# Kernel optimization log

Measured on AMD Instinct MI355X. Metric: run time of the kernel, lower is better.

Reference implementation:

```python
import jax, jax.numpy as jnp
import numpy as np

DIM = 256
KEY_DIM = 16
NUM_HEADS = 8
ATTN_RATIO = 4
NH_KD = KEY_DIM * NUM_HEADS   # 128
D = ATTN_RATIO * KEY_DIM      # 64
DH = D * NUM_HEADS            # 512
POS_LEN = 16
SCALE = KEY_DIM ** -0.5


def _cbn(x, w, s, b):
    # 1x1 conv (no bias) + folded BatchNorm affine. w: [out,in], x: [B,in,H,W]
    y = jnp.einsum('oi,bihw->bohw', w, x)
    return y * s[None, :, None, None] + b[None, :, None, None]


def _interp_pos(pos, n):
    # F.interpolate(mode='linear', align_corners=False) from length POS_LEN to n.
    L = pos.shape[-1]
    coords = (jnp.arange(n, dtype=pos.dtype) + 0.5) * (L / n) - 0.5
    coords = jnp.clip(coords, 0.0, L - 1)
    lo = jnp.floor(coords).astype(jnp.int32)
    hi = jnp.minimum(lo + 1, L - 1)
    t = coords - lo.astype(pos.dtype)
    return pos[..., lo] * (1 - t) + pos[..., hi] * t  # [1,C,n]


def _axial_attn(q_emb, k_emb, v_emb, pos_q, pos_k, n):
    # q_emb/k_emb: [B,NH_KD,n], v_emb: [B,DH,n]
    B = q_emb.shape[0]
    q = (q_emb + _interp_pos(pos_q, n)).reshape(B, NUM_HEADS, KEY_DIM, n)
    k = (k_emb + _interp_pos(pos_k, n)).reshape(B, NUM_HEADS, KEY_DIM, n)
    v = v_emb.reshape(B, NUM_HEADS, D, n)
    attn = jnp.einsum('bhcn,bhcm->bhnm', q, k) * SCALE
    attn = jax.nn.softmax(attn, axis=-1)
    xx = jnp.einsum('bhnm,bhdm->bhnd', attn, v)      # [B,NH,n,D]
    return xx.transpose(0, 1, 3, 2).reshape(B, DH, n)  # [B,DH,n]


def _forward(x, wq, sq, bq, wk, sk, bk, wv, sv, bv,
             pos_rowq, pos_rowk, pos_colq, pos_colk,
             w_row, s_row, b_row, w_col, s_col, b_col,
             w_proj, s_proj, b_proj, w_sc, s_sc, b_sc,
             w_dw, s_dw, b_dw, w_pw, s_pw, b_pw):
    B, C, H, W = x.shape
    q = _cbn(x, wq, sq, bq)   # [B,NH_KD,H,W]
    k = _cbn(x, wk, sk, bk)
    v = _cbn(x, wv, sv, bv)   # [B,DH,H,W]

    # row branch (mean over W)
    xx_row = _axial_attn(q.mean(-1), k.mean(-1), v.mean(-1), pos_rowq, pos_rowk, H)
    xx_row = _cbn(jax.nn.relu(xx_row[..., None]), w_row, s_row, b_row)      # [B,DH,H,1]
    # column branch (mean over H)
    xx_col = _axial_attn(q.mean(-2), k.mean(-2), v.mean(-2), pos_colq, pos_colk, W)
    xx_col = _cbn(jax.nn.relu(xx_col[:, :, None, :]), w_col, s_col, b_col)  # [B,DH,1,W]

    attn_out = v + (xx_row + xx_col)
    attn_out = _cbn(jax.nn.relu(attn_out), w_proj, s_proj, b_proj)          # [B,DIM,H,W]

    # gate branch: 1x1 -> dw3x3 -> relu -> 1x1 -> h_sigmoid
    gate = _cbn(x, w_sc, s_sc, b_sc)
    gate = jax.lax.conv_general_dilated(
        gate, w_dw, (1, 1), 'SAME',
        dimension_numbers=('NCHW', 'OIHW', 'NCHW'), feature_group_count=DIM)
    gate = gate * s_dw[None, :, None, None] + b_dw[None, :, None, None]
    gate = jax.nn.relu(gate)
    gate = _cbn(gate, w_pw, s_pw, b_pw)
    gate = jnp.clip(gate + 3.0, 0.0, 6.0) / 6.0  # h_sigmoid
    return gate * attn_out


def setup_inputs() -> dict:
    key = jax.random.key(0)
    ks = jax.random.split(key, 32)
    B, H, W = 16, 64, 64
    nrm = lambda k, sh, sc=0.05: jax.random.normal(k, sh, dtype=jnp.float32) * sc
    inp = {
        'x': nrm(ks[0], (B, DIM, H, W), 1.0),
        'wq': nrm(ks[1], (NH_KD, DIM)), 'sq': 1.0 + nrm(ks[2], (NH_KD,)), 'bq': nrm(ks[3], (NH_KD,)),
        'wk': nrm(ks[4], (NH_KD, DIM)), 'sk': 1.0 + nrm(ks[5], (NH_KD,)), 'bk': nrm(ks[6], (NH_KD,)),
        'wv': nrm(ks[7], (DH, DIM)), 'sv': 1.0 + nrm(ks[8], (DH,)), 'bv': nrm(ks[9], (DH,)),
        'pos_rowq': nrm(ks[10], (1, NH_KD, POS_LEN), 1.0), 'pos_rowk': nrm(ks[11], (1, NH_KD, POS_LEN), 1.0),
        'pos_colq': nrm(ks[12], (1, NH_KD, POS_LEN), 1.0), 'pos_colk': nrm(ks[13], (1, NH_KD, POS_LEN), 1.0),
        'w_row': nrm(ks[14], (DH, DH)), 's_row': 1.0 + nrm(ks[15], (DH,)), 'b_row': nrm(ks[16], (DH,)),
        'w_col': nrm(ks[17], (DH, DH)), 's_col': 1.0 + nrm(ks[18], (DH,)), 'b_col': nrm(ks[19], (DH,)),
        'w_proj': nrm(ks[20], (DIM, DH)), 's_proj': 1.0 + nrm(ks[21], (DIM,)), 'b_proj': nrm(ks[22], (DIM,)),
        'w_sc': nrm(ks[23], (DIM, DIM)), 's_sc': 1.0 + nrm(ks[24], (DIM,)), 'b_sc': nrm(ks[25], (DIM,)),
        'w_dw': nrm(ks[26], (DIM, 1, 3, 3)), 's_dw': 1.0 + nrm(ks[27], (DIM,)), 'b_dw': nrm(ks[28], (DIM,)),
        'w_pw': nrm(ks[29], (DIM, DIM)), 's_pw': 1.0 + nrm(ks[30], (DIM,)), 'b_pw': nrm(ks[31], (DIM,)),
    }
    return inp


def reference(x, wq, sq, bq, wk, sk, bk, wv, sv, bv,
              pos_rowq, pos_rowk, pos_colq, pos_colk,
              w_row, s_row, b_row, w_col, s_col, b_col,
              w_proj, s_proj, b_proj, w_sc, s_sc, b_sc,
              w_dw, s_dw, b_dw, w_pw, s_pw, b_pw):
    return _forward(x, wq, sq, bq, wk, sk, bk, wv, sv, bv,
                    pos_rowq, pos_rowk, pos_colq, pos_colk,
                    w_row, s_row, b_row, w_col, s_col, b_col,
                    w_proj, s_proj, b_proj, w_sc, s_sc, b_sc,
                    w_dw, s_dw, b_dw, w_pw, s_pw, b_pw)
```

## Files before the change

kernel.cpp:

```cpp
#include <hip/hip_runtime.h>
#include <math.h>

typedef unsigned short u16;
typedef unsigned int u32;
typedef short short8 __attribute__((ext_vector_type(8)));
typedef float f32x4 __attribute__((ext_vector_type(4)));

#define Bn 16
#define Cc 256
#define Pp 4096
#define DHc 512
#define PTOT 65536
#define SCALE 0.25f

__device__ __forceinline__ float bf2f(u16 u) {
    return __uint_as_float(((u32)u) << 16);
}
__device__ __forceinline__ u16 f2bf(float f) {
    u32 u = __float_as_uint(f);
    u32 lsb = (u >> 16) & 1u;
    u += 0x7fffu + lsb;
    return (u16)(u >> 16);
}

__device__ __forceinline__ void gload16(const u16* g, u16* l) {
    __builtin_amdgcn_global_load_lds(
        (const __attribute__((address_space(1))) void*)(uintptr_t)g,
        (__attribute__((address_space(3))) void*)(u32)(uintptr_t)l,
        16, 0, 0);
}

__global__ __launch_bounds__(256) void mean_kernel(
    const float* __restrict__ x, u16* __restrict__ xmb) {
    __shared__ float plane[64][65];
    int bc = blockIdx.x;
    int b = bc >> 8, c = bc & 255;
    const float* xp = x + (size_t)bc * Pp;
    int tid = threadIdx.x;
#pragma unroll
    for (int k = 0; k < 16; ++k) {
        int idx = tid + k * 256;
        plane[idx >> 6][idx & 63] = xp[idx];
    }
    __syncthreads();
    if (tid < 64) {
        float s = 0.f;
#pragma unroll
        for (int w = 0; w < 64; ++w) s += plane[tid][w];
        xmb[((size_t)b * 64 + tid) * 256 + c] = f2bf(s * (1.f / 64.f));
    } else if (tid < 128) {
        int w = tid - 64;
        float s = 0.f;
#pragma unroll
        for (int h = 0; h < 64; ++h) s += plane[h][w];
        xmb[((size_t)1024 + b * 64 + w) * 256 + c] = f2bf(s * (1.f / 64.f));
    }
}

__global__ __launch_bounds__(256) void xpose_kernel(
    const float* __restrict__ x, u16* __restrict__ xbf) {
    __shared__ float tile[64][65];
    int pb = blockIdx.x;
    int cb = blockIdx.y;
    int b = blockIdx.z;
    int t = threadIdx.x;
    int p_l = t & 63, c_q = t >> 6;
    const float* xp = x + ((size_t)b * Cc + cb * 64) * Pp + pb * 64;
#pragma unroll
    for (int rr = 0; rr < 16; ++rr) {
        int c_l = rr * 4 + c_q;
        tile[p_l][c_l] = xp[(size_t)c_l * Pp + p_l];
    }
    __syncthreads();
    int c_l2 = t & 63, p_q = t >> 6;
    u16* dst = xbf + ((size_t)b * Pp + pb * 64) * Cc + cb * 64;
#pragma unroll
    for (int rr = 0; rr < 16; ++rr) {
        int p_l2 = rr * 4 + p_q;
        dst[(size_t)p_l2 * Cc + c_l2] = f2bf(tile[p_l2][c_l2]);
    }
}

__global__ __launch_bounds__(256) void wconv_kernel(
    const float* __restrict__ wq, const float* __restrict__ wk, const float* __restrict__ wv,
    const float* __restrict__ wsc, const float* __restrict__ wproj, const float* __restrict__ wpw,
    const float* __restrict__ wrow, const float* __restrict__ wcol,
    const float* __restrict__ wdw,
    u16* __restrict__ wqkvb, u16* __restrict__ wscb,
    u16* __restrict__ wprojb, u16* __restrict__ wpwb,
    u16* __restrict__ wrb, u16* __restrict__ wcb, float* __restrict__ wdwT) {
    int t = blockIdx.x * 256 + threadIdx.x;
    if (t < 2304) wdwT[(t % 9) * 256 + (t / 9)] = wdw[t];
    if (t < 32768) wqkvb[t] = f2bf(wq[t]);
    else if (t < 65536) wqkvb[t] = f2bf(wk[t - 32768]);
    else if (t < 196608) wqkvb[t] = f2bf(wv[t - 65536]);
    else if (t < 262144) wscb[t - 196608] = f2bf(wsc[t - 196608]);
    else if (t < 393216) wprojb[t - 262144] = f2bf(wproj[t - 262144]);
    else if (t < 458752) wpwb[t - 393216] = f2bf(wpw[t - 393216]);
    else if (t < 720896) wrb[t - 458752] = f2bf(wrow[t - 458752]);
    else wcb[t - 720896] = f2bf(wcol[t - 720896]);
}

__device__ __forceinline__ void gemm_mainloop(
    const u16* __restrict__ W, const u16* __restrict__ X, int K,
    int o0, size_t prow0, u16* ldsA, u16* ldsB, f32x4 (&acc)[4][4]) {
    int t = threadIdx.x;
    int w = t >> 6, lane = t & 63;
    int sr = (w << 5) + (lane >> 2);
    int ks = (lane & 3) * 8;
    const u16* gA = W + (size_t)(o0 + sr) * K + ks;
    const u16* gB = X + (prow0 + sr) * K + ks;
    u16* lA = ldsA + sr * 32 + ks;
    u16* lB = ldsB + sr * 32 + ks;
    int wo = (w >> 1) * 64, wp = (w & 1) * 64;
    const u16* fA = ldsA + (wo + (lane & 15)) * 32 + ((lane >> 4) * 8);
    const u16* fB = ldsB + (wp + (lane & 15)) * 32 + ((lane >> 4) * 8);

    for (int k0 = 0; k0 < K; k0 += 32) {
        if (k0) __syncthreads();
        gload16(gA + k0, lA);
        gload16(gA + k0 + (size_t)16 * K, lA + 16 * 32);
        gload16(gB + k0, lB);
        gload16(gB + k0 + (size_t)16 * K, lB + 16 * 32);
        __syncthreads();
        short8 a[4], b[4];
#pragma unroll
        for (int i = 0; i < 4; ++i) a[i] = *(const short8*)(fA + i * 16 * 32);
#pragma unroll
        for (int j = 0; j < 4; ++j) b[j] = *(const short8*)(fB + j * 16 * 32);
#pragma unroll
        for (int i = 0; i < 4; ++i)
#pragma unroll
            for (int j = 0; j < 4; ++j)
                acc[i][j] = __builtin_amdgcn_mfma_f32_16x16x32_bf16(a[i], b[j], acc[i][j], 0, 0, 0);
    }
}

__global__ __launch_bounds__(256) void gemm_qkv(
    const u16* __restrict__ Wb, const u16* __restrict__ X,
    const float* __restrict__ sq, const float* __restrict__ bq,
    const float* __restrict__ sk, const float* __restrict__ bk,
    const float* __restrict__ sv, const float* __restrict__ bv,
    const float* __restrict__ posrq, const float* __restrict__ posrk,
    const float* __restrict__ poscq, const float* __restrict__ posck,
    float* __restrict__ qrow, float* __restrict__ krow, float* __restrict__ vrow,
    float* __restrict__ qcol, float* __restrict__ kcol, float* __restrict__ vcol) {
    __shared__ u16 ldsA[128 * 32];
    __shared__ u16 ldsB[128 * 32];
    f32x4 acc[4][4];
#pragma unroll
    for (int i = 0; i < 4; ++i)
#pragma unroll
        for (int j = 0; j < 4; ++j) acc[i][j] = (f32x4){0.f, 0.f, 0.f, 0.f};
    int o0 = blockIdx.x * 128;
    size_t prow0 = (size_t)blockIdx.y * 128;
    gemm_mainloop(Wb, X, 256, o0, prow0, ldsA, ldsB, acc);

    int lane = threadIdx.x & 63, w = threadIdx.x >> 6;
    int wo = (w >> 1) * 64, wp = (w & 1) * 64;
    int quad = lane >> 4, cn = lane & 15;
#pragma unroll
    for (int j = 0; j < 4; ++j) {
        int p = (int)prow0 + wp + j * 16 + cn;
        int branch = p >> 10, loc = p & 1023;
        int b = loc >> 6, n = loc & 63;
        float coords = 0.25f * (float)n - 0.375f;
        coords = fminf(fmaxf(coords, 0.f), 15.f);
        int lo = (int)floorf(coords);
        int hi = min(lo + 1, 15);
        float tt = coords - (float)lo;
#pragma unroll
        for (int i = 0; i < 4; ++i) {
            int o = o0 + wo + i * 16 + quad * 4;
            if (o < 128) {
                const float* pos = branch ? poscq : posrq;
                float* dst = branch ? qcol : qrow;
#pragma unroll
                for (int r = 0; r < 4; ++r) {
                    int c = o + r;
                    float pv = pos[c * 16 + lo] * (1.f - tt) + pos[c * 16 + hi] * tt;
                    dst[b * 8192 + c * 64 + n] = acc[i][j][r] * sq[c] + bq[c] + pv;
                }
            } else if (o < 256) {
                const float* pos = branch ? posck : posrk;
                float* dst = branch ? kcol : krow;
#pragma unroll
                for (int r = 0; r < 4; ++r) {
                    int c = o - 128 + r;
                    float pv = pos[c * 16 + lo] * (1.f - tt) + pos[c * 16 + hi] * tt;
                    dst[b * 8192 + c * 64 + n] = acc[i][j][r] * sk[c] + bk[c] + pv;
                }
            } else {
                float* dst = branch ? vcol : vrow;
#pragma unroll
                for (int r = 0; r < 4; ++r) {
                    int c = o - 256 + r;
                    dst[b * 32768 + c * 64 + n] = acc[i][j][r] * sv[c] + bv[c];
                }
            }
        }
    }
}

__global__ __launch_bounds__(512, 2) void attn_kernel(
    const float* __restrict__ qr, const float* __restrict__ kr, const float* __restrict__ vr,
    const float* __restrict__ qc, const float* __restrict__ kc, const float* __restrict__ vc,
    u16* __restrict__ xxbf) {
    int branch = blockIdx.y;
    const float* q = branch ? qc : qr;
    const float* k = branch ? kc : kr;
    const float* v = branch ? vc : vr;
    int bh = blockIdx.x;
    int b = bh >> 3, h = bh & 7;
    __shared__ float qs[16][64], ks[16][64], vs[64][64];
    __shared__ float sl[64][65], el[64][65];
    int t = threadIdx.x;
#pragma unroll
    for (int i = t; i < 1024; i += 512) {
        int c = i >> 6, nn = i & 63;
        qs[c][nn] = q[b * 8192 + (h * 16 + c) * 64 + nn];
        ks[c][nn] = k[b * 8192 + (h * 16 + c) * 64 + nn];
    }
#pragma unroll
    for (int i = t; i < 4096; i += 512) {
        int d = i >> 6, nn = i & 63;
        vs[d][nn] = v[b * 32768 + (h * 64 + d) * 64 + nn];
    }
    __syncthreads();

    int n = t & 63, dq = t >> 6;
    float qv[16];
#pragma unroll
    for (int c = 0; c < 16; ++c) qv[c] = qs[c][n];

    float sp[8];
#pragma unroll
    for (int mm = 0; mm < 8; ++mm) {
        int m = dq * 8 + mm;
        float acc = 0.f;
#pragma unroll
        for (int c = 0; c < 16; ++c) acc += qv[c] * ks[c][m];
        sp[mm] = acc * SCALE;
        sl[n][m] = sp[mm];
    }
    __syncthreads();

    float mx = -1e30f;
#pragma unroll
    for (int m = 0; m < 64; ++m) mx = fmaxf(mx, sl[n][m]);

#pragma unroll
    for (int mm = 0; mm < 8; ++mm) el[n][dq * 8 + mm] = __expf(sp[mm] - mx);
    __syncthreads();

    float sum = 0.f;
#pragma unroll
    for (int m = 0; m < 64; ++m) sum += el[n][m];
    float inv = 1.f / sum;

    float acc[8];
#pragma unroll
    for (int dd = 0; dd < 8; ++dd) acc[dd] = 0.f;
#pragma unroll
    for (int m = 0; m < 64; ++m) {
        float e = el[n][m];
#pragma unroll
        for (int dd = 0; dd < 8; ++dd) acc[dd] += e * vs[dq * 8 + dd][m];
    }
    u16* dst = xxbf + (((size_t)(b * 2 + branch)) * 64 + n) * 512 + h * 64 + dq * 8;
#pragma unroll
    for (int dd = 0; dd < 8; ++dd)
        dst[dd] = f2bf(fmaxf(acc[dd] * inv, 0.f));
}

__global__ __launch_bounds__(256) void post_gemm(
    const u16* __restrict__ xxbf, const u16* __restrict__ wrb, const u16* __restrict__ wcb,
    const float* __restrict__ s_row, const float* __restrict__ b_row,
    const float* __restrict__ s_col, const float* __restrict__ b_col,
    float* __restrict__ xr2, float* __restrict__ xc2) {
    __shared__ u16 ldsA[64 * 32];
    __shared__ u16 ldsB[128 * 32];
    int o0 = blockIdx.x * 128;
    int b = blockIdx.y;
    int branch = blockIdx.z;
    const u16* A = xxbf + ((size_t)(b * 2 + branch)) * 64 * 512;
    const u16* W = branch ? wcb : wrb;
    const float* ss = branch ? s_col : s_row;
    const float* bb = branch ? b_col : b_row;
    float* dst = (branch ? xc2 : xr2) + (size_t)b * 32768;

    f32x4 acc[4][2];
#pragma unroll
    for (int i = 0; i < 4; ++i)
#pragma unroll
        for (int j = 0; j < 2; ++j) acc[i][j] = (f32x4){0.f, 0.f, 0.f, 0.f};

    int t = threadIdx.x, w = t >> 6, lane = t & 63;
    int ks = (t & 3) * 8;
    const u16* gA = A + (size_t)(t >> 2) * 512 + ks;
    const u16* gB = W + (size_t)(o0 + (t >> 2)) * 512 + ks;
    u16* lA = ldsA + (t >> 2) * 32 + ks;
    u16* lB = ldsB + (t >> 2) * 32 + ks;
    const u16* fA = ldsA + (lane & 15) * 32 + ((lane >> 4) * 8);
    const u16* fB = ldsB + (w * 32 + (lane & 15)) * 32 + ((lane >> 4) * 8);

    for (int k0 = 0; k0 < 512; k0 += 32) {
        if (k0) __syncthreads();
        gload16(gA + k0, lA);
#pragma unroll
        for (int r = 0; r < 2; ++r)
            gload16(gB + k0 + (size_t)r * 64 * 512, lB + r * 64 * 32);
        __syncthreads();
        short8 a[4], bfr[2];
#pragma unroll
        for (int i = 0; i < 4; ++i) a[i] = *(const short8*)(fA + i * 16 * 32);
#pragma unroll
        for (int j = 0; j < 2; ++j) bfr[j] = *(const short8*)(fB + j * 16 * 32);
#pragma unroll
        for (int i = 0; i < 4; ++i)
#pragma unroll
            for (int j = 0; j < 2; ++j)
                acc[i][j] = __builtin_amdgcn_mfma_f32_16x16x32_bf16(a[i], bfr[j], acc[i][j], 0, 0, 0);
    }

    int quad = lane >> 4, cn = lane & 15;
#pragma unroll
    for (int i = 0; i < 4; ++i)
#pragma unroll
        for (int j = 0; j < 2; ++j) {
            int o = o0 + w * 32 + j * 16 + cn;
            float sv_ = ss[o], bv_ = bb[o];
#pragma unroll
            for (int r = 0; r < 4; ++r) {
                int n = i * 16 + quad * 4 + r;
                dst[n * 512 + o] = acc[i][j][r] * sv_ + bv_;
            }
        }
}

__global__ __launch_bounds__(256) void gemm_sc(
    const u16* __restrict__ Wb, const u16* __restrict__ X,
    const float* __restrict__ s, const float* __restrict__ bb, u16* __restrict__ outb) {
    __shared__ u16 ldsA[128 * 32];
    __shared__ u16 ldsB[128 * 32];
    f32x4 acc[4][4];
#pragma unroll
    for (int i = 0; i < 4; ++i)
#pragma unroll
        for (int j = 0; j < 4; ++j) acc[i][j] = (f32x4){0.f, 0.f, 0.f, 0.f};
    int o0 = blockIdx.x * 128;
    size_t prow0 = (size_t)blockIdx.y * 128;
    gemm_mainloop(Wb, X, 256, o0, prow0, ldsA, ldsB, acc);

    int lane = threadIdx.x & 63, w = threadIdx.x >> 6;
    int wo = (w >> 1) * 64, wp = (w & 1) * 64;
    int quad = lane >> 4, cn = lane & 15;
#pragma unroll
    for (int i = 0; i < 4; ++i) {
        int ob = o0 + wo + i * 16 + quad * 4;
        f32x4 s4 = *(const f32x4*)&s[ob];
        f32x4 b4 = *(const f32x4*)&bb[ob];
#pragma unroll
        for (int j = 0; j < 4; ++j) {
            size_t p = prow0 + wp + j * 16 + cn;
            ushort4 o4;
            o4.x = f2bf(acc[i][j][0] * s4[0] + b4[0]);
            o4.y = f2bf(acc[i][j][1] * s4[1] + b4[1]);
            o4.z = f2bf(acc[i][j][2] * s4[2] + b4[2]);
            o4.w = f2bf(acc[i][j][3] * s4[3] + b4[3]);
            *(ushort4*)&outb[p * 256 + ob] = o4;
        }
    }
}

__global__ __launch_bounds__(512, 4) void fused_dwpw(
    const u16* __restrict__ sc, const float* __restrict__ wdwT,
    const float* __restrict__ sdw, const float* __restrict__ bdw,
    const u16* __restrict__ Wpw,
    const float* __restrict__ spw, const float* __restrict__ bpw,
    u16* __restrict__ gate) {
    __shared__ u16 dwt[64 * 256];

    int t = threadIdx.x;
    int lane = t & 63, w = t >> 6;
    int quad = lane >> 4, cn = lane & 15;
    int p0 = blockIdx.x * 64;
    int h = (p0 >> 6) & 63;

#pragma unroll
    for (int kq = 0; kq < 4; ++kq) {
        int task = t + kq * 512;
        int p_l = task >> 5;
        int cg = (task & 31) * 8;
        size_t p = (size_t)p0 + p_l;
        float acc[8] = {0.f, 0.f, 0.f, 0.f, 0.f, 0.f, 0.f, 0.f};
#pragma unroll
        for (int ky = 0; ky < 3; ++ky) {
            int hh = h + ky - 1;
            if (hh < 0 || hh > 63) continue;
#pragma unroll
            for (int kx = 0; kx < 3; ++kx) {
                int wx = p_l + kx - 1;
                if (wx < 0 || wx > 63) continue;
                size_t pp = (size_t)((long long)p + (ky - 1) * 64 + (kx - 1));
                short8 v = *(const short8*)&sc[pp * 256 + cg];
                const float* wt = &wdwT[(ky * 3 + kx) * 256 + cg];
                f32x4 w0 = *(const f32x4*)wt;
                f32x4 w1 = *(const f32x4*)(wt + 4);
                acc[0] += w0[0] * bf2f((u16)v[0]); acc[1] += w0[1] * bf2f((u16)v[1]);
                acc[2] += w0[2] * bf2f((u16)v[2]); acc[3] += w0[3] * bf2f((u16)v[3]);
                acc[4] += w1[0] * bf2f((u16)v[4]); acc[5] += w1[1] * bf2f((u16)v[5]);
                acc[6] += w1[2] * bf2f((u16)v[6]); acc[7] += w1[3] * bf2f((u16)v[7]);
            }
        }
        f32x4 s0 = *(const f32x4*)&sdw[cg], s1 = *(const f32x4*)&sdw[cg + 4];
        f32x4 b0 = *(const f32x4*)&bdw[cg], b1 = *(const f32x4*)&bdw[cg + 4];
        short8 o;
        o[0] = (short)f2bf(fmaxf(acc[0] * s0[0] + b0[0], 0.f));
        o[1] = (short)f2bf(fmaxf(acc[1] * s0[1] + b0[1], 0.f));
        o[2] = (short)f2bf(fmaxf(acc[2] * s0[2] + b0[2], 0.f));
        o[3] = (short)f2bf(fmaxf(acc[3] * s0[3] + b0[3], 0.f));
        o[4] = (short)f2bf(fmaxf(acc[4] * s1[0] + b1[0], 0.f));
        o[5] = (short)f2bf(fmaxf(acc[5] * s1[1] + b1[1], 0.f));
        o[6] = (short)f2bf(fmaxf(acc[6] * s1[2] + b1[2], 0.f));
        o[7] = (short)f2bf(fmaxf(acc[7] * s1[3] + b1[3], 0.f));
        int ko = cg >> 3;
        *(short8*)&dwt[p_l * 256 + ((ko ^ (p_l & 7)) << 3)] = o;
    }
    __syncthreads();

    f32x4 acc2[2][4];
#pragma unroll
    for (int i = 0; i < 2; ++i)
#pragma unroll
        for (int j = 0; j < 4; ++j) acc2[i][j] = (f32x4){0.f, 0.f, 0.f, 0.f};

    int ow = w * 32;
    const u16* gA = Wpw + (size_t)(ow + cn) * 256 + quad * 8;

    for (int k0 = 0; k0 < 256; k0 += 32) {
        short8 a[2], b[4];
        a[0] = *(const short8*)(gA + k0);
        a[1] = *(const short8*)(gA + (size_t)16 * 256 + k0);
        int og = (k0 >> 3) + quad;
#pragma unroll
        for (int j = 0; j < 4; ++j) {
            int pl = j * 16 + cn;
            b[j] = *(const short8*)&dwt[pl * 256 + ((og ^ (pl & 7)) << 3)];
        }
#pragma unroll
        for (int i = 0; i < 2; ++i)
#pragma unroll
            for (int j = 0; j < 4; ++j)
                acc2[i][j] = __builtin_amdgcn_mfma_f32_16x16x32_bf16(a[i], b[j], acc2[i][j], 0, 0, 0);
    }

#pragma unroll
    for (int i = 0; i < 2; ++i) {
        int ob = ow + i * 16 + quad * 4;
        f32x4 s4 = *(const f32x4*)&spw[ob];
        f32x4 b4 = *(const f32x4*)&bpw[ob];
#pragma unroll
        for (int j = 0; j < 4; ++j) {
            size_t p = (size_t)p0 + j * 16 + cn;
            ushort4 o4;
            o4.x = f2bf(fminf(fmaxf(acc2[i][j][0] * s4[0] + b4[0] + 3.f, 0.f), 6.f) * (1.f / 6.f));
            o4.y = f2bf(fminf(fmaxf(acc2[i][j][1] * s4[1] + b4[1] + 3.f, 0.f), 6.f) * (1.f / 6.f));
            o4.z = f2bf(fminf(fmaxf(acc2[i][j][2] * s4[2] + b4[2] + 3.f, 0.f), 6.f) * (1.f / 6.f));
            o4.w = f2bf(fminf(fmaxf(acc2[i][j][3] * s4[3] + b4[3] + 3.f, 0.f), 6.f) * (1.f / 6.f));
            *(ushort4*)&gate[p * 256 + ob] = o4;
        }
    }
}

__global__ __launch_bounds__(512, 4) void fused_vproj(
    const u16* __restrict__ Wv, const u16* __restrict__ Wp,
    const u16* __restrict__ X,
    const float* __restrict__ sv, const float* __restrict__ bv,
    const float* __restrict__ xr2, const float* __restrict__ xc2,
    const float* __restrict__ sp, const float* __restrict__ bp,
    const u16* __restrict__ gate, float* __restrict__ out) {
    __shared__ u16 lds[64 * 512];

    int t = threadIdx.x;
    int lane = t & 63, w = t >> 6;
    int quad = lane >> 4, cn = lane & 15;
    int p0 = blockIdx.x * 64;
    int bi = p0 >> 12;
    int hh = (p0 >> 6) & 63;

#pragma unroll
    for (int r = 0; r < 4; ++r) {
        int li = r * 512 + t;
        int p = li >> 5, ko = li & 31;
        gload16(X + ((size_t)(p0 + p)) * 256 + ((ko ^ (p & 7)) << 3),
                lds + (size_t)li * 8);
    }
    __syncthreads();

    f32x4 acc1[4][4];
#pragma unroll
    for (int i = 0; i < 4; ++i)
#pragma unroll
        for (int j = 0; j < 4; ++j) acc1[i][j] = (f32x4){0.f, 0.f, 0.f, 0.f};

    int ow = w * 64;
    const u16* gA = Wv + (size_t)(ow + cn) * 256 + quad * 8;

    short8 a_c[4];
#pragma unroll
    for (int i = 0; i < 4; ++i) a_c[i] = *(const short8*)(gA + (size_t)i * 16 * 256);

#pragma unroll
    for (int kk = 0; kk < 8; ++kk) {
        int k0 = kk * 32;
        short8 a_n[4];
        if (kk < 7) {
#pragma unroll
            for (int i = 0; i < 4; ++i)
                a_n[i] = *(const short8*)(gA + (size_t)i * 16 * 256 + k0 + 32);
        }
        int og = (k0 >> 3) + quad;
        short8 b[4];
#pragma unroll
        for (int j = 0; j < 4; ++j) {
            int pl = j * 16 + cn;
            b[j] = *(const short8*)&lds[pl * 256 + ((og ^ (pl & 7)) << 3)];
        }
#pragma unroll
        for (int i = 0; i < 4; ++i)
#pragma unroll
            for (int j = 0; j < 4; ++j)
                acc1[i][j] = __builtin_amdgcn_mfma_f32_16x16x32_bf16(a_c[i], b[j], acc1[i][j], 0, 0, 0);
        if (kk < 7) {
#pragma unroll
            for (int i = 0; i < 4; ++i) a_c[i] = a_n[i];
        }
    }

    __syncthreads();

#pragma unroll
    for (int i = 0; i < 4; ++i) {
        int ob = ow + i * 16 + quad * 4;
        f32x4 s4 = *(const f32x4*)&sv[ob];
        f32x4 b4 = *(const f32x4*)&bv[ob];
        f32x4 ra = *(const f32x4*)&xr2[(size_t)bi * 32768 + hh * 512 + ob];
#pragma unroll
        for (int j = 0; j < 4; ++j) {
            int p = j * 16 + cn;
            f32x4 ca = *(const f32x4*)&xc2[(size_t)bi * 32768 + p * 512 + ob];
            ushort4 o4;
            o4.x = f2bf(fmaxf(acc1[i][j][0] * s4[0] + b4[0] + ra[0] + ca[0], 0.f));
            o4.y = f2bf(fmaxf(acc1[i][j][1] * s4[1] + b4[1] + ra[1] + ca[1], 0.f));
            o4.z = f2bf(fmaxf(acc1[i][j][2] * s4[2] + b4[2] + ra[2] + ca[2], 0.f));
            o4.w = f2bf(fmaxf(acc1[i][j][3] * s4[3] + b4[3] + ra[3] + ca[3], 0.f));
            *(ushort4*)&lds[p * 512 + (ob ^ ((p & 7) << 3))] = o4;
        }
    }
    __syncthreads();

    f32x4 acc2[2][4];
#pragma unroll
    for (int i = 0; i < 2; ++i)
#pragma unroll
        for (int j = 0; j < 4; ++j) acc2[i][j] = (f32x4){0.f, 0.f, 0.f, 0.f};

    int o2w = w * 32;
    const u16* gP = Wp + (size_t)(o2w + cn) * 512 + quad * 8;

    short8 a2_c[2], b2_c[4];
#pragma unroll
    for (int i = 0; i < 2; ++i) a2_c[i] = *(const short8*)(gP + (size_t)i * 16 * 512);
    {
        int kk0 = quad * 8;
#pragma unroll
        for (int j = 0; j < 4; ++j) {
            int p = j * 16 + cn;
            b2_c[j] = *(const short8*)&lds[p * 512 + (kk0 ^ ((p & 7) << 3))];
        }
    }

#pragma unroll
    for (int kk = 0; kk < 16; ++kk) {
        short8 a2_n[2], b2_n[4];
        if (kk < 15) {
            int k1 = kk * 32 + 32;
#pragma unroll
            for (int i = 0; i < 2; ++i)
                a2_n[i] = *(const short8*)(gP + (size_t)i * 16 * 512 + k1);
            int kn = k1 + quad * 8;
#pragma unroll
            for (int j = 0; j < 4; ++j) {
                int p = j * 16 + cn;
                b2_n[j] = *(const short8*)&lds[p * 512 + (kn ^ ((p & 7) << 3))];
            }
        }
#pragma unroll
        for (int i = 0; i < 2; ++i)
#pragma unroll
            for (int j = 0; j < 4; ++j)
                acc2[i][j] = __builtin_amdgcn_mfma_f32_16x16x32_bf16(a2_c[i], b2_c[j], acc2[i][j], 0, 0, 0);
        if (kk < 15) {
#pragma unroll
            for (int i = 0; i < 2; ++i) a2_c[i] = a2_n[i];
#pragma unroll
            for (int j = 0; j < 4; ++j) b2_c[j] = b2_n[j];
        }
    }

    int pl0 = p0 & 4095;
#pragma unroll
    for (int i = 0; i < 2; ++i) {
        int ob = o2w + i * 16 + quad * 4;
        f32x4 s4 = *(const f32x4*)&sp[ob];
        f32x4 b4 = *(const f32x4*)&bp[ob];
#pragma unroll
        for (int j = 0; j < 4; ++j) {
            int p = j * 16 + cn;
            size_t pg = (size_t)p0 + p;
            ushort4 gv = *(const ushort4*)&gate[pg * 256 + ob];
            float* op = out + (size_t)bi * 1048576 + (size_t)ob * 4096 + (pl0 + p);
            op[0 * 4096] = bf2f(gv.x) * (acc2[i][j][0] * s4[0] + b4[0]);
            op[1 * 4096] = bf2f(gv.y) * (acc2[i][j][1] * s4[1] + b4[1]);
            op[2 * 4096] = bf2f(gv.z) * (acc2[i][j][2] * s4[2] + b4[2]);
            op[3 * 4096] = bf2f(gv.w) * (acc2[i][j][3] * s4[3] + b4[3]);
        }
    }
}

extern "C" void kernel_launch(void* const* d_in, const int* in_sizes, int n_in,
                              void* d_out, int out_size, void* d_ws, size_t ws_size,
                              hipStream_t stream) {
    const float* x = (const float*)d_in[0];
    const float* wq = (const float*)d_in[1];
    const float* sq = (const float*)d_in[2];
    const float* bq = (const float*)d_in[3];
    const float* wk = (const float*)d_in[4];
    const float* sk = (const float*)d_in[5];
    const float* bk = (const float*)d_in[6];
    const float* wv = (const float*)d_in[7];
    const float* sv = (const float*)d_in[8];
    const float* bv = (const float*)d_in[9];
    const float* posrq = (const float*)d_in[10];
    const float* posrk = (const float*)d_in[11];
    const float* poscq = (const float*)d_in[12];
    const float* posck = (const float*)d_in[13];
    const float* w_row = (const float*)d_in[14];
    const float* s_row = (const float*)d_in[15];
    const float* b_row = (const float*)d_in[16];
    const float* w_col = (const float*)d_in[17];
    const float* s_col = (const float*)d_in[18];
    const float* b_col = (const float*)d_in[19];
    const float* w_proj = (const float*)d_in[20];
    const float* s_proj = (const float*)d_in[21];
    const float* b_proj = (const float*)d_in[22];
    const float* w_sc = (const float*)d_in[23];
    const float* s_sc = (const float*)d_in[24];
    const float* b_sc = (const float*)d_in[25];
    const float* w_dw = (const float*)d_in[26];
    const float* s_dw = (const float*)d_in[27];
    const float* b_dw = (const float*)d_in[28];
    const float* w_pw = (const float*)d_in[29];
    const float* s_pw = (const float*)d_in[30];
    const float* b_pw = (const float*)d_in[31];
    float* out = (float*)d_out;

    float* fws = (float*)d_ws;
    float* qrow = fws;
    float* krow = qrow + 131072;
    float* qcol = krow + 131072;
    float* kcol = qcol + 131072;
    float* vrow = kcol + 131072;
    float* vcol = vrow + 524288;
    float* xr2  = vcol + 524288;
    float* xc2  = xr2 + 524288;
    float* wdwT = xc2 + 524288;
    u16* xmb    = (u16*)(wdwT + 2304);
    u16* xbf    = xmb + 524288;
    u16* wqkvb  = xbf + (size_t)PTOT * 256;
    u16* wscb   = wqkvb + 196608;
    u16* wprojb = wscb + 65536;
    u16* wpwb   = wprojb + 131072;
    u16* wrb    = wpwb + 65536;
    u16* wcb    = wrb + 262144;
    u16* xxbf   = wcb + 262144;
    u16* scb    = xxbf + 1048576;
    u16* gate   = scb + (size_t)PTOT * 256;

    mean_kernel<<<dim3(Bn * Cc), 256, 0, stream>>>(x, xmb);
    xpose_kernel<<<dim3(64, 4, Bn), 256, 0, stream>>>(x, xbf);
    wconv_kernel<<<dim3(3840), 256, 0, stream>>>(
        wq, wk, wv, w_sc, w_proj, w_pw, w_row, w_col, w_dw,
        wqkvb, wscb, wprojb, wpwb, wrb, wcb, wdwT);
    gemm_qkv<<<dim3(6, 16), 256, 0, stream>>>(
        wqkvb, xmb, sq, bq, sk, bk, sv, bv,
        posrq, posrk, poscq, posck, qrow, krow, vrow, qcol, kcol, vcol);
    attn_kernel<<<dim3(128, 2), 512, 0, stream>>>(qrow, krow, vrow, qcol, kcol, vcol, xxbf);
    post_gemm<<<dim3(4, Bn, 2), 256, 0, stream>>>(
        xxbf, wrb, wcb, s_row, b_row, s_col, b_col, xr2, xc2);
    gemm_sc<<<dim3(2, 512), 256, 0, stream>>>(wscb, xbf, s_sc, b_sc, scb);
    fused_dwpw<<<dim3(1024), 512, 0, stream>>>(
        scb, wdwT, s_dw, b_dw, wpwb, s_pw, b_pw, gate);
    fused_vproj<<<dim3(1024), 512, 0, stream>>>(
        wqkvb + 65536, wprojb, xbf, sv, bv, xr2, xc2, s_proj, b_proj, gate, out);
}
```

Measured before the change: 391.1 us.

## Fuse shortcut 1x1 conv GEMM into depthwise+pointwise kernel, recomputing halo rows

Removes the separate gemm_sc kernel and its bf16 intermediate buffer. Each 64-pixel row block now recomputes the shortcut conv for its own row and the two neighbouring rows in LDS, then accumulates the 3x3 depthwise conv from LDS. This avoids writing and re-reading the 32 MB sc tensor in global memory. The cost is roughly three times the shortcut GEMM FLOPs, extra barriers, and a larger LDS footprint that may lower occupancy.

```diff
diff --git a/kernel.cpp b/kernel.cpp
--- a/kernel.cpp
+++ b/kernel.cpp
@@ -338,47 +338,15 @@
         }
 }
 
-__global__ __launch_bounds__(256) void gemm_sc(
-    const u16* __restrict__ Wb, const u16* __restrict__ X,
-    const float* __restrict__ s, const float* __restrict__ bb, u16* __restrict__ outb) {
-    __shared__ u16 ldsA[128 * 32];
-    __shared__ u16 ldsB[128 * 32];
-    f32x4 acc[4][4];
-#pragma unroll
-    for (int i = 0; i < 4; ++i)
-#pragma unroll
-        for (int j = 0; j < 4; ++j) acc[i][j] = (f32x4){0.f, 0.f, 0.f, 0.f};
-    int o0 = blockIdx.x * 128;
-    size_t prow0 = (size_t)blockIdx.y * 128;
-    gemm_mainloop(Wb, X, 256, o0, prow0, ldsA, ldsB, acc);
-
-    int lane = threadIdx.x & 63, w = threadIdx.x >> 6;
-    int wo = (w >> 1) * 64, wp = (w & 1) * 64;
-    int quad = lane >> 4, cn = lane & 15;
-#pragma unroll
-    for (int i = 0; i < 4; ++i) {
-        int ob = o0 + wo + i * 16 + quad * 4;
-        f32x4 s4 = *(const f32x4*)&s[ob];
-        f32x4 b4 = *(const f32x4*)&bb[ob];
-#pragma unroll
-        for (int j = 0; j < 4; ++j) {
-            size_t p = prow0 + wp + j * 16 + cn;
-            ushort4 o4;
-            o4.x = f2bf(acc[i][j][0] * s4[0] + b4[0]);
-            o4.y = f2bf(acc[i][j][1] * s4[1] + b4[1]);
-            o4.z = f2bf(acc[i][j][2] * s4[2] + b4[2]);
-            o4.w = f2bf(acc[i][j][3] * s4[3] + b4[3]);
-            *(ushort4*)&outb[p * 256 + ob] = o4;
-        }
-    }
-}
-
-__global__ __launch_bounds__(512, 4) void fused_dwpw(
-    const u16* __restrict__ sc, const float* __restrict__ wdwT,
-    const float* __restrict__ sdw, const float* __restrict__ bdw,
+__global__ __launch_bounds__(512, 4) void fused_scdwpw(
+    const u16* __restrict__ Wsc, const u16* __restrict__ X,
+    const float* __restrict__ ssc, const float* __restrict__ bsc,
+    const float* __restrict__ wdwT, const float* __restrict__ sdw,
+    const float* __restrict__ bdw,
     const u16* __restrict__ Wpw,
     const float* __restrict__ spw, const float* __restrict__ bpw,
     u16* __restrict__ gate) {
+    __shared__ u16 xbuf[64 * 256];
     __shared__ u16 dwt[64 * 256];
 
     int t = threadIdx.x;
@@ -386,44 +354,115 @@
     int quad = lane >> 4, cn = lane & 15;
     int p0 = blockIdx.x * 64;
     int h = (p0 >> 6) & 63;
+    int ow = w * 32;
+
+    float dwacc[4][8];
+#pragma unroll
+    for (int kq = 0; kq < 4; ++kq)
+#pragma unroll
+        for (int e = 0; e < 8; ++e) dwacc[kq][e] = 0.f;
+
+    for (int ky = 0; ky < 3; ++ky) {
+        int hh = h + ky - 1;
+        if (hh < 0 || hh > 63) continue;
+        int pr0 = p0 + (ky - 1) * 64;
+
+#pragma unroll
+        for (int r = 0; r < 4; ++r) {
+            int li = r * 512 + t;
+            int p = li >> 5, ko = li & 31;
+            gload16(X + ((size_t)(pr0 + p)) * 256 + ((ko ^ (p & 7)) << 3),
+                    xbuf + (size_t)li * 8);
+        }
+        __syncthreads();
+
+        f32x4 acc[2][4];
+#pragma unroll
+        for (int i = 0; i < 2; ++i)
+#pragma unroll
+            for (int j = 0; j < 4; ++j) acc[i][j] = (f32x4){0.f, 0.f, 0.f, 0.f};
+
+        const u16* gA = Wsc + (size_t)(ow + cn) * 256 + quad * 8;
+        for (int k0 = 0; k0 < 256; k0 += 32) {
+            short8 a[2], b[4];
+            a[0] = *(const short8*)(gA + k0);
+            a[1] = *(const short8*)(gA + (size_t)16 * 256 + k0);
+            int og = (k0 >> 3) + quad;
+#pragma unroll
+            for (int j = 0; j < 4; ++j) {
+                int pl = j * 16 + cn;
+                b[j] = *(const short8*)&xbuf[pl * 256 + ((og ^ (pl & 7)) << 3)];
+            }
+#pragma unroll
+            for (int i = 0; i < 2; ++i)
+#pragma unroll
+                for (int j = 0; j < 4; ++j)
+                    acc[i][j] = __builtin_amdgcn_mfma_f32_16x16x32_bf16(a[i], b[j], acc[i][j], 0, 0, 0);
+        }
+        __syncthreads();
+
+#pragma unroll
+        for (int i = 0; i < 2; ++i) {
+            int ob = ow + i * 16 + quad * 4;
+            f32x4 s4 = *(const f32x4*)&ssc[ob];
+            f32x4 b4 = *(const f32x4*)&bsc[ob];
+#pragma unroll
+            for (int j = 0; j < 4; ++j) {
+                int p = j * 16 + cn;
+                ushort4 o4;
+                o4.x = f2bf(acc[i][j][0] * s4[0] + b4[0]);
+                o4.y = f2bf(acc[i][j][1] * s4[1] + b4[1]);
+                o4.z = f2bf(acc[i][j][2] * s4[2] + b4[2]);
+                o4.w = f2bf(acc[i][j][3] * s4[3] + b4[3]);
+                int addr = p * 256 + ((((ob >> 3) ^ (p & 7))) << 3) + (ob & 7);
+                *(ushort4*)&xbuf[addr] = o4;
+            }
+        }
+        __syncthreads();
+
+#pragma unroll
+        for (int kq = 0; kq < 4; ++kq) {
+            int task = t + kq * 512;
+            int p_l = task >> 5;
+            int cg = (task & 31) * 8;
+            int ko = cg >> 3;
+#pragma unroll
+            for (int kx = 0; kx < 3; ++kx) {
+                int wx = p_l + kx - 1;
+                if (wx < 0 || wx > 63) continue;
+                short8 v = *(const short8*)&xbuf[wx * 256 + ((ko ^ (wx & 7)) << 3)];
+                const float* wt = &wdwT[(ky * 3 + kx) * 256 + cg];
+                f32x4 w0 = *(const f32x4*)wt;
+                f32x4 w1 = *(const f32x4*)(wt + 4);
+                dwacc[kq][0] += w0[0] * bf2f((u16)v[0]);
+                dwacc[kq][1] += w0[1] * bf2f((u16)v[1]);
+                dwacc[kq][2] += w0[2] * bf2f((u16)v[2]);
+                dwacc[kq][3] += w0[3] * bf2f((u16)v[3]);
+                dwacc[kq][4] += w1[0] * bf2f((u16)v[4]);
+                dwacc[kq][5] += w1[1] * bf2f((u16)v[5]);
+                dwacc[kq][6] += w1[2] * bf2f((u16)v[6]);
+                dwacc[kq][7] += w1[3] * bf2f((u16)v[7]);
+            }
+        }
+        __syncthreads();
+    }
 
 #pragma unroll
     for (int kq = 0; kq < 4; ++kq) {
         int task = t + kq * 512;
         int p_l = task >> 5;
         int cg = (task & 31) * 8;
-        size_t p = (size_t)p0 + p_l;
-        float acc[8] = {0.f, 0.f, 0.f, 0.f, 0.f, 0.f, 0.f, 0.f};
-#pragma unroll
-        for (int ky = 0; ky < 3; ++ky) {
-            int hh = h + ky - 1;
-            if (hh < 0 || hh > 63) continue;
-#pragma unroll
-            for (int kx = 0; kx < 3; ++kx) {
-                int wx = p_l + kx - 1;
-                if (wx < 0 || wx > 63) continue;
-                size_t pp = (size_t)((long long)p + (ky - 1) * 64 + (kx - 1));
-                short8 v = *(const short8*)&sc[pp * 256 + cg];
-                const float* wt = &wdwT[(ky * 3 + kx) * 256 + cg];
-                f32x4 w0 = *(const f32x4*)wt;
-                f32x4 w1 = *(const f32x4*)(wt + 4);
-                acc[0] += w0[0] * bf2f((u16)v[0]); acc[1] += w0[1] * bf2f((u16)v[1]);
-                acc[2] += w0[2] * bf2f((u16)v[2]); acc[3] += w0[3] * bf2f((u16)v[3]);
-                acc[4] += w1[0] * bf2f((u16)v[4]); acc[5] += w1[1] * bf2f((u16)v[5]);
-                acc[6] += w1[2] * bf2f((u16)v[6]); acc[7] += w1[3] * bf2f((u16)v[7]);
-            }
-        }
         f32x4 s0 = *(const f32x4*)&sdw[cg], s1 = *(const f32x4*)&sdw[cg + 4];
         f32x4 b0 = *(const f32x4*)&bdw[cg], b1 = *(const f32x4*)&bdw[cg + 4];
         short8 o;
-        o[0] = (short)f2bf(fmaxf(acc[0] * s0[0] + b0[0], 0.f));
-        o[1] = (short)f2bf(fmaxf(acc[1] * s0[1] + b0[1], 0.f));
-        o[2] = (short)f2bf(fmaxf(acc[2] * s0[2] + b0[2], 0.f));
-        o[3] = (short)f2bf(fmaxf(acc[3] * s0[3] + b0[3], 0.f));
-        o[4] = (short)f2bf(fmaxf(acc[4] * s1[0] + b1[0], 0.f));
-        o[5] = (short)f2bf(fmaxf(acc[5] * s1[1] + b1[1], 0.f));
-        o[6] = (short)f2bf(fmaxf(acc[6] * s1[2] + b1[2], 0.f));
-        o[7] = (short)f2bf(fmaxf(acc[7] * s1[3] + b1[3], 0.f));
+        o[0] = (short)f2bf(fmaxf(dwacc[kq][0] * s0[0] + b0[0], 0.f));
+        o[1] = (short)f2bf(fmaxf(dwacc[kq][1] * s0[1] + b0[1], 0.f));
+        o[2] = (short)f2bf(fmaxf(dwacc[kq][2] * s0[2] + b0[2], 0.f));
+        o[3] = (short)f2bf(fmaxf(dwacc[kq][3] * s0[3] + b0[3], 0.f));
+        o[4] = (short)f2bf(fmaxf(dwacc[kq][4] * s1[0] + b1[0], 0.f));
+        o[5] = (short)f2bf(fmaxf(dwacc[kq][5] * s1[1] + b1[1], 0.f));
+        o[6] = (short)f2bf(fmaxf(dwacc[kq][6] * s1[2] + b1[2], 0.f));
+        o[7] = (short)f2bf(fmaxf(dwacc[kq][7] * s1[3] + b1[3], 0.f));
         int ko = cg >> 3;
         *(short8*)&dwt[p_l * 256 + ((ko ^ (p_l & 7)) << 3)] = o;
     }
@@ -435,13 +474,11 @@
 #pragma unroll
         for (int j = 0; j < 4; ++j) acc2[i][j] = (f32x4){0.f, 0.f, 0.f, 0.f};
 
-    int ow = w * 32;
-    const u16* gA = Wpw + (size_t)(ow + cn) * 256 + quad * 8;
-
+    const u16* gP = Wpw + (size_t)(ow + cn) * 256 + quad * 8;
     for (int k0 = 0; k0 < 256; k0 += 32) {
         short8 a[2], b[4];
-        a[0] = *(const short8*)(gA + k0);
-        a[1] = *(const short8*)(gA + (size_t)16 * 256 + k0);
+        a[0] = *(const short8*)(gP + k0);
+        a[1] = *(const short8*)(gP + (size_t)16 * 256 + k0);
         int og = (k0 >> 3) + quad;
 #pragma unroll
         for (int j = 0; j < 4; ++j) {
@@ -685,8 +722,7 @@
     u16* wrb    = wpwb + 65536;
     u16* wcb    = wrb + 262144;
     u16* xxbf   = wcb + 262144;
-    u16* scb    = xxbf + 1048576;
-    u16* gate   = scb + (size_t)PTOT * 256;
+    u16* gate   = xxbf + 1048576;
 
     mean_kernel<<<dim3(Bn * Cc), 256, 0, stream>>>(x, xmb);
     xpose_kernel<<<dim3(64, 4, Bn), 256, 0, stream>>>(x, xbf);
@@ -699,9 +735,8 @@
     attn_kernel<<<dim3(128, 2), 512, 0, stream>>>(qrow, krow, vrow, qcol, kcol, vcol, xxbf);
     post_gemm<<<dim3(4, Bn, 2), 256, 0, stream>>>(
         xxbf, wrb, wcb, s_row, b_row, s_col, b_col, xr2, xc2);
-    gemm_sc<<<dim3(2, 512), 256, 0, stream>>>(wscb, xbf, s_sc, b_sc, scb);
-    fused_dwpw<<<dim3(1024), 512, 0, stream>>>(
-        scb, wdwT, s_dw, b_dw, wpwb, s_pw, b_pw, gate);
+    fused_scdwpw<<<dim3(1024), 512, 0, stream>>>(
+        wscb, xbf, s_sc, b_sc, wdwT, s_dw, b_dw, wpwb, s_pw, b_pw, gate);
     fused_vproj<<<dim3(1024), 512, 0, stream>>>(
         wqkvb + 65536, wprojb, xbf, sv, bv, xr2, xc2, s_proj, b_proj, gate, out);
 }
```

After: 432.8 us. +10.7%, slower.
